# Performance work log

Hardware: AMD Instinct MI355X
Metric: run time of the kernel (lower is better)

Reference implementation:

```python
import jax, jax.numpy as jnp
import numpy as np

B, T, D = 4, 1024, 1024
H = 16
DH = D // H  # 64
NEG = jnp.float32(-2.0**32 + 1)


def _sinusoid_table(T, D):
    pos = np.arange(T)[:, None]
    i = np.arange(D)[None, :]
    angle = pos / np.power(10000.0, 2.0 * (i // 2) / D)
    tab = np.zeros((T, D))
    tab[:, 0::2] = np.sin(angle[:, 0::2])
    tab[:, 1::2] = np.cos(angle[:, 1::2])
    return jnp.asarray(tab, dtype=jnp.float32)


def setup_inputs() -> dict:
    key = jax.random.key(0)
    ks = jax.random.split(key, 10)
    inp = {
        "queries": jax.random.normal(ks[0], (B, T, D), dtype=jnp.float32),
        "keys": jax.random.normal(ks[1], (B, T, D), dtype=jnp.float32),
        "query_lens": jax.random.randint(ks[2], (B, 1), 1, T + 1),
        "key_lens": jax.random.randint(ks[3], (B, 1), 1, T + 1),
        # learned params
        "pe_q": _sinusoid_table(T, D),
        "pe_k": _sinusoid_table(T, D),
        "W_Query": jax.random.truncated_normal(ks[4], -2.0, 2.0, (D, D), dtype=jnp.float32) * 0.05,
        "W_key": jax.random.truncated_normal(ks[5], -2.0, 2.0, (D, D), dtype=jnp.float32) * 0.05,
        "W_Value": jax.random.truncated_normal(ks[6], -2.0, 2.0, (D, D), dtype=jnp.float32) * 0.05,
        "fw1": jax.random.normal(ks[7], (D, 4 * D), dtype=jnp.float32) * (1.0 / np.sqrt(D)),
        "fw2": jax.random.normal(ks[8], (4 * D, D), dtype=jnp.float32) * (1.0 / np.sqrt(4 * D)),
    }
    return inp


def _forward(queries, keys, pe_q, pe_k, W_Query, W_key, W_Value, fw1, fw2,
             query_lens, key_lens):
    scale = jnp.float32(np.sqrt(D))
    # positional encoding (scale=True). NOTE: source bug preserved —
    # keys tensor is overwritten by key_pe applied to the PE'd queries.
    q_in = queries + pe_q[None] * scale          # [B,T,D]
    k_in = q_in + pe_k[None] * scale             # [B,T,D]

    Q = q_in @ W_Query                           # [B,T,D]
    K = k_in @ W_key                             # [B,T,D]
    V = K @ W_Value                              # NOTE: V projected from projected keys (source quirk)

    def heads(x):  # [B,T,D] -> [H,B,T,DH]
        return x.reshape(B, T, H, DH).transpose(2, 0, 1, 3)

    Qh, Kh, Vh = heads(Q), heads(K), heads(V)
    scores = jnp.einsum("hbqd,hbkd->hbqk", Qh, Kh) / jnp.float32(np.sqrt(DH))

    t = jnp.arange(T)
    kmask = (t[None, :] < key_lens).astype(jnp.float32)    # [B,T]
    qmask = (t[None, :] < query_lens).astype(jnp.float32)  # [B,T]

    scores = jnp.where(kmask[None, :, None, :] == 1.0, scores, NEG)
    # blinding: set diagonal to large negative
    eye = jnp.eye(T, dtype=bool)
    scores = jnp.where(eye[None, None], NEG, scores)

    scores = scores - scores.max(axis=-1, keepdims=True)
    probs = jax.nn.softmax(scores, axis=-1)
    probs = probs * qmask[None, :, :, None]

    out = jnp.einsum("hbqk,hbkd->hbqd", probs, Vh)         # [H,B,T,DH]
    result = out.transpose(1, 2, 0, 3).reshape(B, T, D)
    result = result + q_in                                  # residual uses PE'd queries

    ff = jnp.maximum(result @ fw1, 0.0) @ fw2
    result = result + ff
    return result.mean(axis=1, keepdims=True)               # [B,1,D]


def reference(queries, keys, query_lens, key_lens, pe_q, pe_k,
              W_Query, W_key, W_Value, fw1, fw2):
    return _forward(queries, keys, pe_q, pe_k, W_Query, W_key, W_Value,
                    fw1, fw2, query_lens, key_lens)
```

## Files before the change

### kernel.cpp

```cpp
#include <hip/hip_runtime.h>

#define T_ 1024
#define D_ 1024
#define B_ 4
#define H_ 16
#define DH_ 64
#define M_ (B_*T_)
#define NEG_ (-4294967295.0f)

typedef __attribute__((ext_vector_type(8))) _Float16 f16x8;
typedef __attribute__((ext_vector_type(4))) float f32x4;

__device__ __forceinline__ unsigned short f2h(float f) {
    _Float16 h = (_Float16)f; unsigned short u; __builtin_memcpy(&u, &h, 2); return u;
}
__device__ __forceinline__ float h2f(unsigned short u) {
    _Float16 h; __builtin_memcpy(&h, &u, 2); return (float)h;
}

typedef const unsigned int __attribute__((address_space(1)))* gas_p;
typedef unsigned int __attribute__((address_space(3)))* las_p;
__device__ __forceinline__ void gl_lds16(const void* g, void* l) {
    __builtin_amdgcn_global_load_lds((gas_p)g, (las_p)l, 16, 0, 0);
}

__global__ __launch_bounds__(256) void conv_all(const float* __restrict__ q,
                                                const float* __restrict__ peq,
                                                const float* __restrict__ pek,
                                                const float* __restrict__ Wq,
                                                const float* __restrict__ Wk,
                                                const float* __restrict__ Wv,
                                                const float* __restrict__ fw1,
                                                unsigned short* __restrict__ A2,
                                                unsigned short* __restrict__ B2,
                                                unsigned short* __restrict__ WvT,
                                                unsigned short* __restrict__ fw1T)
{
    int blk = blockIdx.x;
    if (blk < 8192) {
        int i = blk * 256 + threadIdx.x;
        int m = i >> 8, c4 = (i & 255) << 2;
        int mq = m & 4095;
        float4 qv = *(const float4*)(q + (size_t)mq * D_ + c4);
        float4 p  = *(const float4*)(peq + (size_t)(m & (T_-1)) * D_ + c4);
        ushort4 h;
        if (m < 4096) {
            h.x = f2h(qv.x + 32.f*p.x); h.y = f2h(qv.y + 32.f*p.y);
            h.z = f2h(qv.z + 32.f*p.z); h.w = f2h(qv.w + 32.f*p.w);
        } else {
            float4 pk = *(const float4*)(pek + (size_t)(m & (T_-1)) * D_ + c4);
            h.x = f2h(qv.x + 32.f*(p.x + pk.x)); h.y = f2h(qv.y + 32.f*(p.y + pk.y));
            h.z = f2h(qv.z + 32.f*(p.z + pk.z)); h.w = f2h(qv.w + 32.f*(p.w + pk.w));
        }
        *(ushort4*)(A2 + (size_t)m * 1024 + c4) = h;
        return;
    }
    __shared__ float t[32][33];
    int r = threadIdx.x >> 5, c = threadIdx.x & 31;
    if (blk < 10240) {
        int l = blk - 8192;
        int z = l >> 10, k0 = ((l >> 5) & 31) * 32, n0 = (l & 31) * 32;
        const float* W = z ? Wk : Wq;
        #pragma unroll
        for (int rr = 0; rr < 4; ++rr)
            t[r + 8*rr][c] = W[(size_t)(k0 + r + 8*rr) * 1024 + n0 + c];
        __syncthreads();
        #pragma unroll
        for (int rr = 0; rr < 4; ++rr)
            B2[(size_t)(z * 1024 + n0 + r + 8*rr) * 1024 + k0 + c] = f2h(t[c][r + 8*rr]);
    } else if (blk < 11264) {
        int l = blk - 10240;
        int k0 = (l >> 5) * 32, n0 = (l & 31) * 32;
        #pragma unroll
        for (int rr = 0; rr < 4; ++rr)
            t[r + 8*rr][c] = Wv[(size_t)(k0 + r + 8*rr) * 1024 + n0 + c];
        __syncthreads();
        #pragma unroll
        for (int rr = 0; rr < 4; ++rr)
            WvT[(size_t)(n0 + r + 8*rr) * 1024 + k0 + c] = f2h(t[c][r + 8*rr]);
    } else {
        int l = blk - 11264;
        int k0 = (l >> 7) * 32, n0 = (l & 127) * 32;
        #pragma unroll
        for (int rr = 0; rr < 4; ++rr)
            t[r + 8*rr][c] = fw1[(size_t)(k0 + r + 8*rr) * 4096 + n0 + c];
        __syncthreads();
        #pragma unroll
        for (int rr = 0; rr < 4; ++rr)
            fw1T[(size_t)(n0 + r + 8*rr) * 1024 + k0 + c] = f2h(t[c][r + 8*rr]);
    }
}

template<int BM>
__global__ __launch_bounds__(256) void gemm_mfma(
    const unsigned short* __restrict__ A, int lda,
    const unsigned short* __restrict__ B, int ldb, int K,
    float* __restrict__ outf,
    unsigned short* __restrict__ outh, unsigned short* __restrict__ outh2,
    int N, int flags,
    const int* __restrict__ qlv, const int* __restrict__ klv,
    float* __restrict__ hpart)
{
    constexpr int WN = (BM == 128) ? 2 : 4;
    constexpr int FN = 8 / WN;
    constexpr int NA = BM / 32;
    __shared__ __align__(16) unsigned short As[2][BM * 64];
    __shared__ __align__(16) unsigned short Bs[2][128 * 64];
    __shared__ float hp[4][64];
    const int tid = threadIdx.x;
    const int m0 = blockIdx.y * BM, n0 = blockIdx.x << 7;
    if (flags & 32) {
        if (m0 < 4096) {
            if (n0 >= 1024) return;
            if ((m0 & 1023) >= qlv[m0 >> 10]) return;
        } else {
            if (n0 < 1024) return;
            if ((m0 & 1023) >= klv[(m0 - 4096) >> 10]) return;
        }
    }
    if (flags & 256) {
        int bb = m0 >> 10, kl = klv[bb];
        if (kl > 1 && (m0 & 1023) >= kl) return;
    }
    const int lane = tid & 63, wave = tid >> 6;
    const int wm = (wave / WN) * 64;
    const int wn = (wave % WN) * (128 / WN);
    const int rl = lane & 15, kg = lane >> 4;
    const int rl7 = lane & 7;

    int ca[NA]; const unsigned short* gA[NA];
    #pragma unroll
    for (int i = 0; i < NA; ++i) {
        int c = i * 256 + tid;
        int row = c >> 3, k8 = (c & 7) ^ (row & 7);
        ca[i] = c * 8;
        gA[i] = A + (size_t)(m0 + row) * lda + k8 * 8;
    }
    int cb[4]; const unsigned short* gB[4];
    #pragma unroll
    for (int i = 0; i < 4; ++i) {
        int c = i * 256 + tid;
        int row = c >> 3, k8 = (c & 7) ^ (row & 7);
        cb[i] = c * 8;
        gB[i] = B + (size_t)(n0 + row) * ldb + k8 * 8;
    }

    int aoff[2][4], boff[2][FN];
    #pragma unroll
    for (int tt = 0; tt < 2; ++tt) {
        #pragma unroll
        for (int f = 0; f < 4; ++f)
            aoff[tt][f] = (wm + (f << 4) + rl) * 64 + (((tt * 4 + kg) ^ rl7) << 3);
        #pragma unroll
        for (int f = 0; f < FN; ++f)
            boff[tt][f] = (wn + (f << 4) + rl) * 64 + (((tt * 4 + kg) ^ rl7) << 3);
    }

    f32x4 acc[4][FN];
    #pragma unroll
    for (int i = 0; i < 4; ++i)
        #pragma unroll
        for (int j = 0; j < FN; ++j) {
            acc[i][j][0] = 0.f; acc[i][j][1] = 0.f;
            acc[i][j][2] = 0.f; acc[i][j][3] = 0.f;
        }

    const int NT = K >> 6;
    #pragma unroll
    for (int i = 0; i < 4; ++i)  gl_lds16(gB[i], &Bs[0][cb[i]]);
    #pragma unroll
    for (int i = 0; i < NA; ++i) gl_lds16(gA[i], &As[0][ca[i]]);
    #pragma unroll
    for (int i = 0; i < 4; ++i)  gl_lds16(gB[i] + 64, &Bs[1][cb[i]]);
    #pragma unroll
    for (int i = 0; i < NA; ++i) gl_lds16(gA[i] + 64, &As[1][ca[i]]);

    for (int t = 0; t < NT; ++t) {
        const int cur = t & 1;
        if (t + 1 < NT) {
            if constexpr (BM == 128) asm volatile("s_waitcnt vmcnt(8)" ::: "memory");
            else                     asm volatile("s_waitcnt vmcnt(6)" ::: "memory");
        } else {
            asm volatile("s_waitcnt vmcnt(0)" ::: "memory");
        }
        __builtin_amdgcn_s_barrier();
        __builtin_amdgcn_sched_barrier(0);
        f16x8 av[2][4], bv[2][FN];
        #pragma unroll
        for (int tt = 0; tt < 2; ++tt) {
            #pragma unroll
            for (int f = 0; f < 4; ++f)
                av[tt][f] = *(const f16x8*)&As[cur][aoff[tt][f]];
            #pragma unroll
            for (int f = 0; f < FN; ++f)
                bv[tt][f] = *(const f16x8*)&Bs[cur][boff[tt][f]];
        }
        asm volatile("s_waitcnt lgkmcnt(0)" ::: "memory");
        __builtin_amdgcn_sched_barrier(0);
        __builtin_amdgcn_s_barrier();
        __builtin_amdgcn_sched_barrier(0);
        if (t + 2 < NT) {
            const int ko = (t + 2) << 6;
            #pragma unroll
            for (int i = 0; i < 4; ++i)  gl_lds16(gB[i] + ko, &Bs[cur][cb[i]]);
            #pragma unroll
            for (int i = 0; i < NA; ++i) gl_lds16(gA[i] + ko, &As[cur][ca[i]]);
        }
        #pragma unroll
        for (int fm = 0; fm < 4; ++fm)
            #pragma unroll
            for (int fn = 0; fn < FN; ++fn) {
                acc[fm][fn] = __builtin_amdgcn_mfma_f32_16x16x32_f16(av[0][fm], bv[0][fn], acc[fm][fn], 0, 0, 0);
                acc[fm][fn] = __builtin_amdgcn_mfma_f32_16x16x32_f16(av[1][fm], bv[1][fn], acc[fm][fn], 0, 0, 0);
            }
    }

    if (flags & 128) {
        if constexpr (BM == 128) {
            #pragma unroll
            for (int fn = 0; fn < FN; ++fn) {
                float p = 0.f;
                #pragma unroll
                for (int fm = 0; fm < 4; ++fm)
                    #pragma unroll
                    for (int r = 0; r < 4; ++r) p += fmaxf(acc[fm][fn][r], 0.f);
                p += __shfl_xor(p, 16);
                p += __shfl_xor(p, 32);
                if (kg == 0) hp[wave][fn * 16 + rl] = p;
            }
            __syncthreads();
            if (tid < 128) {
                int c = tid;
                float s = (c < 64) ? (hp[0][c] + hp[2][c]) : (hp[1][c - 64] + hp[3][c - 64]);
                hpart[(size_t)blockIdx.y * 4096 + n0 + c] = s;
            }
        }
        return;
    }

    #pragma unroll
    for (int fm = 0; fm < 4; ++fm) {
        int row = m0 + wm + (fm << 4) + (kg << 2);
        #pragma unroll
        for (int fn = 0; fn < FN; ++fn) {
            int col = n0 + wn + (fn << 4) + rl;
            if (flags & 64) {
                ushort4 u;
                u.x = f2h(acc[fm][fn][0]); u.y = f2h(acc[fm][fn][1]);
                u.z = f2h(acc[fm][fn][2]); u.w = f2h(acc[fm][fn][3]);
                size_t a = ((size_t)((row >> 10) * 16 + (col >> 6)) * 64 + (col & 63)) * 1024 + (row & 1023);
                *(ushort4*)(outh + a) = u;
                continue;
            }
            #pragma unroll
            for (int r = 0; r < 4; ++r) {
                float x = acc[fm][fn][r];
                int rr = row + r;
                if (flags & 32) {
                    if (rr < 4096) outh[(size_t)rr * 1024 + col] = f2h(x);
                    else           outh2[(size_t)(rr - 4096) * 1024 + (col - 1024)] = f2h(x);
                } else {
                    size_t idx = (size_t)rr * N + col;
                    if (flags & 1)  x = fmaxf(x, 0.f);
                    if (flags & 8)  outf[idx] = x;
                    if (flags & 16) outh[idx] = f2h(x);
                }
            }
        }
    }
}

__global__ __launch_bounds__(256) void attn_mfma(
    const unsigned short* __restrict__ Qh,
    const unsigned short* __restrict__ Kh,
    const unsigned short* __restrict__ Vt,
    unsigned short* __restrict__ q16,
    const int* __restrict__ qlens, const int* __restrict__ klens)
{
    __shared__ __align__(16) unsigned short KS[4096];
    __shared__ __align__(16) unsigned short VtS[4096];
    __shared__ __align__(16) unsigned short Pl[4][1152];

    const int tid = threadIdx.x;
    const int bh = blockIdx.x & 63;
    const int qt = blockIdx.x >> 6;
    const int b = bh >> 4, h = bh & 15;
    const int qbase = qt * 64;
    const int qlen = qlens[b], klen = klens[b];
    if (qbase >= qlen) return;

    const int lane = tid & 63, wq = tid >> 6;
    const int rl = lane & 15, kg = lane >> 4, rl7 = lane & 7;
    const int gq = qbase + wq * 16 + rl;

    f16x8 qb[2];
    {
        const unsigned short* p1 = Qh + (size_t)(b * 1024 + gq) * 1024 + h * 64 + kg * 8;
        qb[0] = *(const f16x8*)p1;  qb[1] = *(const f16x8*)(p1 + 32);
    }

    const unsigned short* gK[2]; const unsigned short* gV[2];
    int cs[2];
    #pragma unroll
    for (int i = 0; i < 2; ++i) {
        int c = i * 256 + tid;
        int row = c >> 3, ch = (c & 7) ^ (row & 7);
        cs[i] = c * 8;
        gK[i] = Kh + (size_t)(b * 1024 + row) * 1024 + h * 64 + ch * 8;
        gV[i] = Vt + (size_t)(bh * 64 + row) * 1024 + ch * 8;
    }

    int akoff[4][2];
    #pragma unroll
    for (int mf = 0; mf < 4; ++mf)
        #pragma unroll
        for (int kh = 0; kh < 2; ++kh)
            akoff[mf][kh] = (mf * 16 + rl) * 64 + (((kg + 4 * kh) ^ rl7) << 3);

    f32x4 o[4];
    #pragma unroll
    for (int i = 0; i < 4; ++i) { o[i][0]=0.f; o[i][1]=0.f; o[i][2]=0.f; o[i][3]=0.f; }
    float m_run = -3.0e38f, l_run = 0.f;
    const int nt = (klen == 1) ? (T_ / 64) : ((klen + 63) >> 6);

    for (int kb = 0; kb < nt; ++kb) {
        const int kbase = kb * 64;
        const size_t koff = (size_t)kbase * 1024;
        gl_lds16(gK[0] + koff, &KS[cs[0]]);
        gl_lds16(gK[1] + koff, &KS[cs[1]]);
        gl_lds16(gV[0] + kbase, &VtS[cs[0]]);
        gl_lds16(gV[1] + kbase, &VtS[cs[1]]);
        __syncthreads();

        float v[4][4];
        __builtin_amdgcn_s_setprio(1);
        #pragma unroll
        for (int mf = 0; mf < 4; ++mf) {
            f32x4 s; s[0]=0.f; s[1]=0.f; s[2]=0.f; s[3]=0.f;
            f16x8 a0 = *(const f16x8*)&KS[akoff[mf][0]];
            f16x8 a1 = *(const f16x8*)&KS[akoff[mf][1]];
            s = __builtin_amdgcn_mfma_f32_16x16x32_f16(a0, qb[0], s, 0, 0, 0);
            s = __builtin_amdgcn_mfma_f32_16x16x32_f16(a1, qb[1], s, 0, 0, 0);
            #pragma unroll
            for (int r = 0; r < 4; ++r) {
                int gk = kbase + mf * 16 + kg * 4 + r;
                float x = s[r] * 0.125f;
                if (gk >= klen || gk == gq) x = NEG_;
                v[mf][r] = x;
            }
        }
        __builtin_amdgcn_s_setprio(0);
        float mt = -3.0e38f;
        #pragma unroll
        for (int mf = 0; mf < 4; ++mf)
            #pragma unroll
            for (int r = 0; r < 4; ++r) mt = fmaxf(mt, v[mf][r]);
        mt = fmaxf(mt, __shfl_xor(mt, 16));
        mt = fmaxf(mt, __shfl_xor(mt, 32));
        float mnew = fmaxf(m_run, mt);
        float fac = __expf(m_run - mnew);
        float sum = 0.f;
        #pragma unroll
        for (int mf = 0; mf < 4; ++mf) {
            ushort4 pb;
            pb.x = f2h(__expf(v[mf][0] - mnew));
            pb.y = f2h(__expf(v[mf][1] - mnew));
            pb.z = f2h(__expf(v[mf][2] - mnew));
            pb.w = f2h(__expf(v[mf][3] - mnew));
            sum += h2f(pb.x) + h2f(pb.y) + h2f(pb.z) + h2f(pb.w);
            *(ushort4*)&Pl[wq][rl * 72 + mf * 16 + kg * 4] = pb;
        }
        sum += __shfl_xor(sum, 16);
        sum += __shfl_xor(sum, 32);
        l_run = l_run * fac + sum;
        m_run = mnew;
        #pragma unroll
        for (int i = 0; i < 4; ++i) {
            o[i][0] *= fac; o[i][1] *= fac; o[i][2] *= fac; o[i][3] *= fac;
        }
        f16x8 bp0 = *(const f16x8*)&Pl[wq][rl * 72 + kg * 8];
        f16x8 bp1 = *(const f16x8*)&Pl[wq][rl * 72 + 32 + kg * 8];
        __builtin_amdgcn_s_setprio(1);
        #pragma unroll
        for (int dmf = 0; dmf < 4; ++dmf) {
            f16x8 a0 = *(const f16x8*)&VtS[akoff[dmf][0]];
            f16x8 a1 = *(const f16x8*)&VtS[akoff[dmf][1]];
            o[dmf] = __builtin_amdgcn_mfma_f32_16x16x32_f16(a0, bp0, o[dmf], 0, 0, 0);
            o[dmf] = __builtin_amdgcn_mfma_f32_16x16x32_f16(a1, bp1, o[dmf], 0, 0, 0);
        }
        __builtin_amdgcn_s_setprio(0);
        __syncthreads();
    }

    float invl = (gq < qlen) ? (1.f / l_run) : 0.f;
    #pragma unroll
    for (int dmf = 0; dmf < 4; ++dmf)
        #pragma unroll
        for (int r = 0; r < 4; ++r) {
            int dh = dmf * 16 + kg * 4 + r;
            size_t a = (size_t)(b * 1024 + gq) * 1024 + h * 64 + dh;
            q16[a] = f2h(o[dmf][r] * invl + h2f(q16[a]));
        }
}

__global__ __launch_bounds__(256) void mean16(const unsigned short* __restrict__ X,
                                              float* __restrict__ out, int Xdim)
{
    __shared__ float red[4][128];
    int tid = threadIdx.x;
    int b = blockIdx.y;
    int dbase = blockIdx.x * 128;
    int tq = tid >> 6, dd = tid & 63;
    int d = dbase + dd * 2;
    const unsigned short* p = X + ((size_t)b * T_ + tq * 256) * Xdim + d;
    float s0 = 0.f, s1 = 0.f;
    for (int t = 0; t < 256; ++t) {
        ushort2 v = *(const ushort2*)(p + (size_t)t * Xdim);
        s0 += h2f(v.x); s1 += h2f(v.y);
    }
    red[tq][dd*2] = s0; red[tq][dd*2 + 1] = s1;
    __syncthreads();
    if (tq == 0) {
        float a = red[0][dd*2] + red[1][dd*2] + red[2][dd*2] + red[3][dd*2];
        float c = red[0][dd*2+1] + red[1][dd*2+1] + red[2][dd*2+1] + red[3][dd*2+1];
        out[(size_t)b * Xdim + d]     = a * (1.f/1024.f);
        out[(size_t)b * Xdim + d + 1] = c * (1.f/1024.f);
    }
}

__global__ __launch_bounds__(256) void final_partial(const float* __restrict__ Hpart,
                                                     const float* __restrict__ fw2,
                                                     float* __restrict__ Pout)
{
    __shared__ float red[4][4][64];
    __shared__ float hm[4][128];
    int tid = threadIdx.x;
    #pragma unroll
    for (int s = 0; s < 2; ++s) {
        int idx = s * 256 + tid;
        int bb = idx >> 7, jl = idx & 127;
        int j = blockIdx.y * 128 + jl;
        float acc = 0.f;
        #pragma unroll
        for (int i = 0; i < 8; ++i)
            acc += Hpart[((size_t)(bb * 8 + i)) * 4096 + j];
        hm[bb][jl] = acc * (1.f / 1024.f);
    }
    __syncthreads();
    int dd = tid & 63;
    int d = blockIdx.x * 64 + dd;
    int jq = tid >> 6;
    float s4[4] = {0.f, 0.f, 0.f, 0.f};
    for (int jj = 0; jj < 32; ++jj) {
        int jl = jq * 32 + jj;
        int j = blockIdx.y * 128 + jl;
        float wv = fw2[(size_t)j * 1024 + d];
        s4[0] += hm[0][jl] * wv;
        s4[1] += hm[1][jl] * wv;
        s4[2] += hm[2][jl] * wv;
        s4[3] += hm[3][jl] * wv;
    }
    #pragma unroll
    for (int bb = 0; bb < 4; ++bb) red[jq][bb][dd] = s4[bb];
    __syncthreads();
    if (jq == 0) {
        #pragma unroll
        for (int bb = 0; bb < 4; ++bb) {
            float tot = red[0][bb][dd] + red[1][bb][dd] + red[2][bb][dd] + red[3][bb][dd];
            Pout[((size_t)blockIdx.y * 4 + bb) * 1024 + d] = tot;
        }
    }
}

__global__ __launch_bounds__(256) void reduce_out(const float* __restrict__ Mres,
                                                  const float* __restrict__ Pout,
                                                  float* __restrict__ out)
{
    int idx = blockIdx.x * 256 + threadIdx.x;
    int b = idx >> 10, d = idx & 1023;
    float s = Mres[(size_t)b * 1024 + d];
    #pragma unroll
    for (int jy = 0; jy < 32; ++jy)
        s += Pout[((size_t)jy * 4 + b) * 1024 + d];
    out[(size_t)b * 1024 + d] = s;
}

extern "C" void kernel_launch(void* const* d_in, const int* in_sizes, int n_in,
                              void* d_out, int out_size, void* d_ws, size_t ws_size,
                              hipStream_t stream)
{
    const float* queries = (const float*)d_in[0];
    const int*   qlens   = (const int*)d_in[2];
    const int*   klens   = (const int*)d_in[3];
    const float* pe_q    = (const float*)d_in[4];
    const float* pe_k    = (const float*)d_in[5];
    const float* Wq      = (const float*)d_in[6];
    const float* Wk      = (const float*)d_in[7];
    const float* Wv      = (const float*)d_in[8];
    const float* fw1     = (const float*)d_in[9];
    const float* fw2     = (const float*)d_in[10];
    float* out = (float*)d_out;

    char* w = (char*)d_ws;
    unsigned short* Qh   = (unsigned short*)(w);
    unsigned short* A2   = (unsigned short*)(w + (8ll  << 20));
    unsigned short* q16  = A2;
    unsigned short* Kh16 = (unsigned short*)(w + (24ll << 20));
    unsigned short* B2   = (unsigned short*)(w + (32ll << 20));
    unsigned short* WvT  = (unsigned short*)(w + (36ll << 20));
    unsigned short* Vt   = (unsigned short*)(w + (38ll << 20));
    unsigned short* fw1T = (unsigned short*)(w + (46ll << 20));
    float*          Hpart= (float*)(w + (54ll << 20));
    float*          Mres = (float*)(w + (55ll << 20));
    float*          Pout = (float*)(w + (56ll << 20));

    conv_all<<<15360, 256, 0, stream>>>(queries, pe_q, pe_k, Wq, Wk, Wv, fw1,
                                        A2, B2, WvT, fw1T);
    gemm_mfma<128><<<dim3(16, 64), 256, 0, stream>>>(
        A2, 1024, B2, 1024, 1024,
        nullptr, Qh, Kh16, 2048, 32, qlens, klens, nullptr);
    gemm_mfma<64><<<dim3(8, 64), 256, 0, stream>>>(
        Kh16, 1024, WvT, 1024, 1024,
        nullptr, Vt, nullptr, 1024, 64 | 256, nullptr, klens, nullptr);
    attn_mfma<<<1024, 256, 0, stream>>>(Qh, Kh16, Vt, q16, qlens, klens);
    gemm_mfma<128><<<dim3(32, 32), 256, 0, stream>>>(
        q16, 1024, fw1T, 1024, 1024,
        nullptr, nullptr, nullptr, 4096, 128, nullptr, nullptr, Hpart);
    mean16<<<dim3(8, 4), 256, 0, stream>>>(q16, Mres, 1024);
    final_partial<<<dim3(16, 32), 256, 0, stream>>>(Hpart, fw2, Pout);
    reduce_out<<<16, 256, 0, stream>>>(Mres, Pout, out);
}
```

Measured before the change: 140.1 us.

## Double-buffer K/V tiles in attention and skip masked key rows in conversion

The attention kernel now keeps two LDS buffers for K and V tiles and prefetches the tile two steps ahead with async global-to-LDS loads, using vmcnt waits and raw barriers instead of a load-then-syncthreads each iteration. The goal is to hide global load latency behind the MFMA and softmax work. The conversion kernel also skips writing key-side input rows beyond the key length, and the GEMM's skip condition is adjusted to keep those rows when klen==1. The cost is twice the LDS for K and V, which may lower occupancy, and the prologue may prefetch a second tile even when only one is needed.

```diff
diff --git a/kernel.cpp b/kernel.cpp
--- a/kernel.cpp
+++ b/kernel.cpp
@@ -31,6 +31,7 @@
                                                 const float* __restrict__ Wk,
                                                 const float* __restrict__ Wv,
                                                 const float* __restrict__ fw1,
+                                                const int* __restrict__ klv,
                                                 unsigned short* __restrict__ A2,
                                                 unsigned short* __restrict__ B2,
                                                 unsigned short* __restrict__ WvT,
@@ -41,6 +42,11 @@
         int i = blk * 256 + threadIdx.x;
         int m = i >> 8, c4 = (i & 255) << 2;
         int mq = m & 4095;
+        if (m >= 4096) {
+            int row = m - 4096;
+            int kl = klv[row >> 10];
+            if (kl > 1 && (row & 1023) >= kl) return;
+        }
         float4 qv = *(const float4*)(q + (size_t)mq * D_ + c4);
         float4 p  = *(const float4*)(peq + (size_t)(m & (T_-1)) * D_ + c4);
         ushort4 h;
@@ -115,7 +121,8 @@
             if ((m0 & 1023) >= qlv[m0 >> 10]) return;
         } else {
             if (n0 < 1024) return;
-            if ((m0 & 1023) >= klv[(m0 - 4096) >> 10]) return;
+            int kl = klv[(m0 - 4096) >> 10];
+            if (kl > 1 && (m0 & 1023) >= kl) return;
         }
     }
     if (flags & 256) {
@@ -277,8 +284,8 @@
     unsigned short* __restrict__ q16,
     const int* __restrict__ qlens, const int* __restrict__ klens)
 {
-    __shared__ __align__(16) unsigned short KS[4096];
-    __shared__ __align__(16) unsigned short VtS[4096];
+    __shared__ __align__(16) unsigned short KS[2][4096];
+    __shared__ __align__(16) unsigned short VtS[2][4096];
     __shared__ __align__(16) unsigned short Pl[4][1152];
 
     const int tid = threadIdx.x;
@@ -323,22 +330,30 @@
     float m_run = -3.0e38f, l_run = 0.f;
     const int nt = (klen == 1) ? (T_ / 64) : ((klen + 63) >> 6);
 
+    gl_lds16(gK[0], &KS[0][cs[0]]);
+    gl_lds16(gK[1], &KS[0][cs[1]]);
+    gl_lds16(gV[0], &VtS[0][cs[0]]);
+    gl_lds16(gV[1], &VtS[0][cs[1]]);
+    gl_lds16(gK[0] + 65536, &KS[1][cs[0]]);
+    gl_lds16(gK[1] + 65536, &KS[1][cs[1]]);
+    gl_lds16(gV[0] + 64,    &VtS[1][cs[0]]);
+    gl_lds16(gV[1] + 64,    &VtS[1][cs[1]]);
+
     for (int kb = 0; kb < nt; ++kb) {
+        const int cur = kb & 1;
         const int kbase = kb * 64;
-        const size_t koff = (size_t)kbase * 1024;
-        gl_lds16(gK[0] + koff, &KS[cs[0]]);
-        gl_lds16(gK[1] + koff, &KS[cs[1]]);
-        gl_lds16(gV[0] + kbase, &VtS[cs[0]]);
-        gl_lds16(gV[1] + kbase, &VtS[cs[1]]);
-        __syncthreads();
+        if (kb + 1 < nt) asm volatile("s_waitcnt vmcnt(4)" ::: "memory");
+        else             asm volatile("s_waitcnt vmcnt(0)" ::: "memory");
+        __builtin_amdgcn_s_barrier();
+        __builtin_amdgcn_sched_barrier(0);
 
         float v[4][4];
         __builtin_amdgcn_s_setprio(1);
         #pragma unroll
         for (int mf = 0; mf < 4; ++mf) {
             f32x4 s; s[0]=0.f; s[1]=0.f; s[2]=0.f; s[3]=0.f;
-            f16x8 a0 = *(const f16x8*)&KS[akoff[mf][0]];
-            f16x8 a1 = *(const f16x8*)&KS[akoff[mf][1]];
+            f16x8 a0 = *(const f16x8*)&KS[cur][akoff[mf][0]];
+            f16x8 a1 = *(const f16x8*)&KS[cur][akoff[mf][1]];
             s = __builtin_amdgcn_mfma_f32_16x16x32_f16(a0, qb[0], s, 0, 0, 0);
             s = __builtin_amdgcn_mfma_f32_16x16x32_f16(a1, qb[1], s, 0, 0, 0);
             #pragma unroll
@@ -383,13 +398,21 @@
         __builtin_amdgcn_s_setprio(1);
         #pragma unroll
         for (int dmf = 0; dmf < 4; ++dmf) {
-            f16x8 a0 = *(const f16x8*)&VtS[akoff[dmf][0]];
-            f16x8 a1 = *(const f16x8*)&VtS[akoff[dmf][1]];
+            f16x8 a0 = *(const f16x8*)&VtS[cur][akoff[dmf][0]];
+            f16x8 a1 = *(const f16x8*)&VtS[cur][akoff[dmf][1]];
             o[dmf] = __builtin_amdgcn_mfma_f32_16x16x32_f16(a0, bp0, o[dmf], 0, 0, 0);
             o[dmf] = __builtin_amdgcn_mfma_f32_16x16x32_f16(a1, bp1, o[dmf], 0, 0, 0);
         }
         __builtin_amdgcn_s_setprio(0);
-        __syncthreads();
+        __builtin_amdgcn_s_barrier();
+        __builtin_amdgcn_sched_barrier(0);
+        if (kb + 2 < nt) {
+            const size_t ko = (size_t)(kbase + 128) * 1024;
+            gl_lds16(gK[0] + ko, &KS[cur][cs[0]]);
+            gl_lds16(gK[1] + ko, &KS[cur][cs[1]]);
+            gl_lds16(gV[0] + kbase + 128, &VtS[cur][cs[0]]);
+            gl_lds16(gV[1] + kbase + 128, &VtS[cur][cs[1]]);
+        }
     }
 
     float invl = (gq < qlen) ? (1.f / l_run) : 0.f;
@@ -514,7 +537,7 @@
     float*          Mres = (float*)(w + (55ll << 20));
     float*          Pout = (float*)(w + (56ll << 20));
 
-    conv_all<<<15360, 256, 0, stream>>>(queries, pe_q, pe_k, Wq, Wk, Wv, fw1,
+    conv_all<<<15360, 256, 0, stream>>>(queries, pe_q, pe_k, Wq, Wk, Wv, fw1, klens,
                                         A2, B2, WvT, fw1T);
     gemm_mfma<128><<<dim3(16, 64), 256, 0, stream>>>(
         A2, 1024, B2, 1024, 1024,
```

Result: faster. 129.6 us (-7.5%).
